# Performance work log

Hardware: AMD Instinct MI355X
Metric: run time of the kernel (lower is better)

Reference implementation:

```python
import jax, jax.numpy as jnp
import numpy as np

B, N, HID = 2, 2048, 1024
NH = 16
HD = HID // NH

def setup_inputs() -> dict:
    key = jax.random.key(0)
    ks = jax.random.split(key, 5)
    s = 0.02
    return {
        "hidden_states": jax.random.normal(ks[0], (B, N, HID), jnp.float32),
        "attention_mask": jnp.zeros((B, 1, 1, N), jnp.float32),
        "Wq": jax.random.normal(ks[1], (HID, HID), jnp.float32) * s,
        "bq": jnp.zeros((HID,), jnp.float32),
        "Wk": jax.random.normal(ks[2], (HID, HID), jnp.float32) * s,
        "bk": jnp.zeros((HID,), jnp.float32),
        "Wv": jax.random.normal(ks[3], (HID, HID), jnp.float32) * s,
        "bv": jnp.zeros((HID,), jnp.float32),
    }

def reference(hidden_states, attention_mask, Wq, bq, Wk, bk, Wv, bv):
    b, n, _ = hidden_states.shape
    def split_heads(t):  # [b,n,hid] -> [b,h,n,d]
        return t.reshape(b, n, NH, HD).transpose(0, 2, 1, 3)
    q = split_heads(hidden_states @ Wq.T + bq)
    k = split_heads(hidden_states @ Wk.T + bk)
    v = split_heads(hidden_states @ Wv.T + bv)
    scores = jnp.einsum('bhnd,bhmd->bhnm', q, k) / jnp.sqrt(jnp.float32(HD)).astype(q.dtype)
    scores = scores + attention_mask
    scores = jnp.maximum(scores, jnp.finfo(scores.dtype).min)
    probs = jax.nn.softmax(scores, axis=-1)
    out = jnp.einsum('bhnm,bhmd->bhnd', probs, v)
    return out.transpose(0, 2, 1, 3).reshape(b, n, NH * HD)
```

## Files before the change

### kernel.cpp

```cpp
#include <hip/hip_runtime.h>

typedef unsigned short u16;
typedef unsigned int   u32;
typedef __attribute__((ext_vector_type(8))) short bf16x8;
typedef __attribute__((ext_vector_type(4))) float f32x4;

__device__ __forceinline__ float bf2f(u16 u) { return __uint_as_float(((u32)u) << 16); }
__device__ __forceinline__ u16 f2bf(float f) {
    return (u16)((__float_as_uint(f) + 0x8000u) >> 16);
}
__device__ __forceinline__ void gload16(const void* g, void* l) {
    __builtin_amdgcn_global_load_lds((const __attribute__((address_space(1))) void*)g,
                                     (__attribute__((address_space(3))) void*)l, 16, 0, 0);
}

struct us4 { u16 x, y, z, w; };
__global__ void cvt_all(const float* __restrict__ hs, const float* __restrict__ wq,
                        const float* __restrict__ wk, const float* __restrict__ wv,
                        u16* __restrict__ dst)
{
    int i = blockIdx.x * blockDim.x + threadIdx.x;
    const int stride = gridDim.x * blockDim.x;
    us4* d4 = (us4*)dst;
    for (; i < 1835008; i += stride) {
        const float4* s4;
        int j = i;
        if (j < 1048576)      { s4 = (const float4*)hs; }
        else if (j < 1310720) { s4 = (const float4*)wq; j -= 1048576; }
        else if (j < 1572864) { s4 = (const float4*)wk; j -= 1310720; }
        else                  { s4 = (const float4*)wv; j -= 1572864; }
        float4 v = s4[j];
        us4 o;
        o.x = f2bf(v.x); o.y = f2bf(v.y); o.z = f2bf(v.z); o.w = f2bf(v.w);
        d4[i] = o;
    }
}

__global__ __launch_bounds__(256) void qkv_gemm(
    const u16* __restrict__ hs,
    const u16* __restrict__ Wq, const u16* __restrict__ Wk, const u16* __restrict__ Wv,
    const float* __restrict__ bq, const float* __restrict__ bk, const float* __restrict__ bv,
    u16* __restrict__ oq, u16* __restrict__ ok, u16* __restrict__ ovt)
{
    __shared__ u16 smem[12288];
    u16* sA = smem;
    u16* sB = smem + 4096;

    const int tid  = threadIdx.x;
    const int lane = tid & 63;
    const int wv_  = tid >> 6;
    const int c15  = lane & 15;
    const int q4   = lane >> 4;
    const int rb   = blockIdx.x;
    const int mat  = blockIdx.y >> 3;
    const int cb   = blockIdx.y & 7;

    const u16*   W    = (mat == 0) ? Wq : (mat == 1 ? Wk : Wv);
    const float* bias = (mat == 0) ? bq : (mat == 1 ? bk : bv);

    f32x4 acc[4][2] = {};

    int rA[2], cA[2], rB[4], cB[4];
#pragma unroll
    for (int p = 0; p < 2; ++p) {
        const int ch = p * 256 + tid;
        rA[p] = ch >> 3; cA[p] = ((ch & 7) ^ (rA[p] & 7)) * 8;
    }
#pragma unroll
    for (int p = 0; p < 4; ++p) {
        const int ch = p * 256 + tid;
        rB[p] = ch >> 3; cB[p] = ((ch & 7) ^ (rB[p] & 7)) * 8;
    }
    const u16* gA = hs + (rb * 64) * 1024;
    const u16* gB = W + (cb * 128) * 1024;
    const int swz = c15 & 7;

    for (int kb = 0; kb < 1024; kb += 64) {
        __syncthreads();
#pragma unroll
        for (int p = 0; p < 2; ++p)
            gload16(gA + rA[p] * 1024 + kb + cA[p], sA + (p * 256 + wv_ * 64) * 8);
#pragma unroll
        for (int p = 0; p < 4; ++p)
            gload16(gB + rB[p] * 1024 + kb + cB[p], sB + (p * 256 + wv_ * 64) * 8);
        __syncthreads();

#pragma unroll
        for (int kk = 0; kk < 2; ++kk) {
            const int cpos = ((kk * 4 + q4) ^ swz) * 8;
            bf16x8 af[4], bf[2];
#pragma unroll
            for (int mt = 0; mt < 4; ++mt)
                af[mt] = *(const bf16x8*)(sA + (mt * 16 + c15) * 64 + cpos);
#pragma unroll
            for (int nt = 0; nt < 2; ++nt)
                bf[nt] = *(const bf16x8*)(sB + (wv_ * 32 + nt * 16 + c15) * 64 + cpos);
#pragma unroll
            for (int mt = 0; mt < 4; ++mt)
#pragma unroll
                for (int nt = 0; nt < 2; ++nt)
                    acc[mt][nt] = __builtin_amdgcn_mfma_f32_16x16x32_bf16(
                        af[mt], bf[nt], acc[mt][nt], 0, 0, 0);
        }
    }

    __syncthreads();
    const int hcol = cb * 2 + (wv_ >> 1);
    const int dbase = (wv_ & 1) * 32;
    float bvv[2];
#pragma unroll
    for (int nt = 0; nt < 2; ++nt)
        bvv[nt] = bias[cb * 128 + wv_ * 32 + nt * 16 + c15];

    u16* sc = smem + wv_ * 2560;
    if (mat != 2) {
        u16* dst = (mat == 0) ? oq : ok;
#pragma unroll
        for (int mt = 0; mt < 4; ++mt)
#pragma unroll
            for (int nt = 0; nt < 2; ++nt)
#pragma unroll
                for (int r = 0; r < 4; ++r)
                    sc[(mt * 16 + q4 * 4 + r) * 40 + nt * 16 + c15] =
                        f2bf(acc[mt][nt][r] + bvv[nt]);
#pragma unroll
        for (int i = 0; i < 4; ++i) {
            const int rl = i * 16 + (lane >> 2);
            const int c0 = (lane & 3) * 8;
            bf16x8 vv = *(const bf16x8*)(sc + rl * 40 + c0);
            const int n = rb * 64 + rl;
            const int bb = n >> 11, nn = n & 2047;
            *(bf16x8*)(dst + (((bb * 16 + hcol) * 2048) + nn) * 64 + dbase + c0) = vv;
        }
    } else {
#pragma unroll
        for (int mt = 0; mt < 4; ++mt)
#pragma unroll
            for (int nt = 0; nt < 2; ++nt)
#pragma unroll
                for (int r = 0; r < 4; ++r)
                    sc[(nt * 16 + c15) * 72 + mt * 16 + q4 * 4 + r] =
                        f2bf(acc[mt][nt][r] + bvv[nt]);
#pragma unroll
        for (int i = 0; i < 4; ++i) {
            const int dp = i * 8 + (lane >> 3);
            const int nl = (lane & 7) * 8;
            bf16x8 vv = *(const bf16x8*)(sc + dp * 72 + nl);
            const int n = rb * 64 + nl;
            const int bb = n >> 11, nn = n & 2047;
            *(bf16x8*)(ovt + (((bb * 16 + hcol) * 64) + dbase + dp) * 2048 + nn) = vv;
        }
    }
}

__global__ __launch_bounds__(256) void attn(
    const u16* __restrict__ qm, const u16* __restrict__ km, const u16* __restrict__ vtm,
    const float* __restrict__ mask, float* __restrict__ out)
{
    __shared__ u16 sK[64 * 64];
    __shared__ u16 sVT[64 * 64];
    __shared__ u16 sP[4][32 * 72];

    const int tid = threadIdx.x, lane = tid & 63, w = tid >> 6;
    const int c15 = lane & 15, q4 = lane >> 4;
    const int qt = blockIdx.x;
    const int bh = blockIdx.y;
    const int b = bh >> 4;

    bf16x8 qf[2][2];
    const u16* qbase = qm + (bh * 2048 + qt * 128 + w * 32) * 64;
#pragma unroll
    for (int rt = 0; rt < 2; ++rt)
#pragma unroll
        for (int kt = 0; kt < 2; ++kt)
            qf[rt][kt] = *(const bf16x8*)(qbase + (rt * 16 + c15) * 64 + kt * 32 + q4 * 8);

    float l_acc[2][4] = {};
    f32x4 accO[2][4] = {};

    const u16* kbase  = km  + bh * 2048 * 64;
    const u16* vtbase = vtm + bh * 64 * 2048;

    const int r0 = tid >> 3,         cc0 = ((tid & 7) ^ (r0 & 7)) * 8;
    const int r1 = (256 + tid) >> 3, cc1 = ((tid & 7) ^ (r1 & 7)) * 8;

    for (int it = 0; it < 32; ++it) {
        const int kb = it * 64;
        __syncthreads();

        gload16(kbase + (kb + r0) * 64 + cc0, sK + (w * 64) * 8);
        gload16(kbase + (kb + r1) * 64 + cc1, sK + (256 + w * 64) * 8);
        gload16(vtbase + r0 * 2048 + kb + cc0, sVT + (w * 64) * 8);
        gload16(vtbase + r1 * 2048 + kb + cc1, sVT + (256 + w * 64) * 8);
        __syncthreads();

        float mk[4];
#pragma unroll
        for (int nt = 0; nt < 4; ++nt)
            mk[nt] = mask[b * 2048 + kb + nt * 16 + c15];

        f32x4 accS[2][4] = {};
#pragma unroll
        for (int kt = 0; kt < 2; ++kt) {
            bf16x8 kf[4];
#pragma unroll
            for (int nt = 0; nt < 4; ++nt) {
                const int key = nt * 16 + c15;
                const int cpos = (q4 + 4 * kt) ^ (key & 7);
                kf[nt] = *(const bf16x8*)(sK + key * 64 + cpos * 8);
            }
#pragma unroll
            for (int rt = 0; rt < 2; ++rt)
#pragma unroll
                for (int nt = 0; nt < 4; ++nt)
                    accS[rt][nt] = __builtin_amdgcn_mfma_f32_16x16x32_bf16(
                        qf[rt][kt], kf[nt], accS[rt][nt], 0, 0, 0);
        }

#pragma unroll
        for (int rt = 0; rt < 2; ++rt)
#pragma unroll
            for (int nt = 0; nt < 4; ++nt)
#pragma unroll
                for (int r = 0; r < 4; ++r) {
                    const float p = __expf(fmaf(accS[rt][nt][r], 0.125f, mk[nt]));
                    l_acc[rt][r] += p;
                    sP[w][(rt * 16 + q4 * 4 + r) * 72 + nt * 16 + c15] = f2bf(p);
                }


#pragma unroll
        for (int kt = 0; kt < 2; ++kt) {
            bf16x8 pf[2], vf[4];
#pragma unroll
            for (int rt = 0; rt < 2; ++rt)
                pf[rt] = *(const bf16x8*)(&sP[w][(rt * 16 + c15) * 72 + kt * 32 + q4 * 8]);
#pragma unroll
            for (int nt = 0; nt < 4; ++nt) {
                const int d = nt * 16 + c15;
                const int cpos = (kt * 4 + q4) ^ (d & 7);
                vf[nt] = *(const bf16x8*)(sVT + d * 64 + cpos * 8);
            }
#pragma unroll
            for (int rt = 0; rt < 2; ++rt)
#pragma unroll
                for (int nt = 0; nt < 4; ++nt)
                    accO[rt][nt] = __builtin_amdgcn_mfma_f32_16x16x32_bf16(
                        pf[rt], vf[nt], accO[rt][nt], 0, 0, 0);
        }
    }

#pragma unroll
    for (int off = 1; off < 16; off <<= 1)
#pragma unroll
        for (int rt = 0; rt < 2; ++rt)
#pragma unroll
            for (int r = 0; r < 4; ++r)
                l_acc[rt][r] += __shfl_xor(l_acc[rt][r], off);

    const int h = bh & 15;
#pragma unroll
    for (int rt = 0; rt < 2; ++rt) {
        float inv[4];
#pragma unroll
        for (int r = 0; r < 4; ++r) inv[r] = 1.0f / l_acc[rt][r];
#pragma unroll
        for (int nt = 0; nt < 4; ++nt)
#pragma unroll
            for (int r = 0; r < 4; ++r) {
                const int qrow = qt * 128 + w * 32 + rt * 16 + q4 * 4 + r;
                const int d = nt * 16 + c15;
                out[(b * 2048 + qrow) * 1024 + h * 64 + d] = accO[rt][nt][r] * inv[r];
            }
    }
}

extern "C" void kernel_launch(void* const* d_in, const int* in_sizes, int n_in,
                              void* d_out, int out_size, void* d_ws, size_t ws_size,
                              hipStream_t stream)
{
    const float* hs   = (const float*)d_in[0];
    const float* mask = (const float*)d_in[1];
    const float* Wq   = (const float*)d_in[2];
    const float* bq   = (const float*)d_in[3];
    const float* Wk   = (const float*)d_in[4];
    const float* bk   = (const float*)d_in[5];
    const float* Wv   = (const float*)d_in[6];
    const float* bv   = (const float*)d_in[7];

    u16* ws   = (u16*)d_ws;
    u16* qw   = ws;
    u16* kw   = ws + 4194304;
    u16* vtw  = ws + 8388608;
    u16* hsb  = ws + 12582912;
    u16* wqb  = ws + 16777216;
    u16* wkb  = ws + 17825792;
    u16* wvb  = ws + 18874368;

    cvt_all<<<1024, 256, 0, stream>>>(hs, Wq, Wk, Wv, hsb);

    qkv_gemm<<<dim3(64, 24), 256, 0, stream>>>(hsb, wqb, wkb, wvb, bq, bk, bv, qw, kw, vtw);
    attn<<<dim3(16, 32), 256, 0, stream>>>(qw, kw, vtw, mask, (float*)d_out);
}
```

Measured before the change: 180.5 us.

## Compute transposed scores and feed probabilities to PV MFMA from registers

Computes S^T = K·Q^T so each lane's accumulator output matches the A-operand layout of the PV MFMA. This drops the per-wave sP shared-memory round trip. Probabilities are packed into bf16 registers with the upper half zero-padded, since only 16 keys per tile are used in the 32-wide MFMA. V^T is loaded as 8-byte halves to match. The padding doubles the PV MFMA count relative to useful work, in exchange for removing LDS writes, reads and related stalls. Row sums now need only two cross-lane shuffles plus a broadcast.

```diff
diff --git a/kernel.cpp b/kernel.cpp
--- a/kernel.cpp
+++ b/kernel.cpp
@@ -4,6 +4,7 @@
 typedef unsigned int   u32;
 typedef __attribute__((ext_vector_type(8))) short bf16x8;
 typedef __attribute__((ext_vector_type(4))) float f32x4;
+typedef __attribute__((ext_vector_type(2))) unsigned int u32x2;
 
 __device__ __forceinline__ float bf2f(u16 u) { return __uint_as_float(((u32)u) << 16); }
 __device__ __forceinline__ u16 f2bf(float f) {
@@ -159,7 +160,6 @@
 {
     __shared__ u16 sK[64 * 64];
     __shared__ u16 sVT[64 * 64];
-    __shared__ u16 sP[4][32 * 72];
 
     const int tid = threadIdx.x, lane = tid & 63, w = tid >> 6;
     const int c15 = lane & 15, q4 = lane >> 4;
@@ -175,7 +175,7 @@
         for (int kt = 0; kt < 2; ++kt)
             qf[rt][kt] = *(const bf16x8*)(qbase + (rt * 16 + c15) * 64 + kt * 32 + q4 * 8);
 
-    float l_acc[2][4] = {};
+    float l_acc[2] = {0.f, 0.f};
     f32x4 accO[2][4] = {};
 
     const u16* kbase  = km  + bh * 2048 * 64;
@@ -194,76 +194,82 @@
         gload16(vtbase + r1 * 2048 + kb + cc1, sVT + (256 + w * 64) * 8);
         __syncthreads();
 
-        float mk[4];
-#pragma unroll
-        for (int nt = 0; nt < 4; ++nt)
-            mk[nt] = mask[b * 2048 + kb + nt * 16 + c15];
-
-        f32x4 accS[2][4] = {};
+        float mkv[4][4];
+#pragma unroll
+        for (int ktile = 0; ktile < 4; ++ktile) {
+            float4 m4 = *(const float4*)(mask + b * 2048 + kb + ktile * 16 + q4 * 4);
+            mkv[ktile][0] = m4.x; mkv[ktile][1] = m4.y;
+            mkv[ktile][2] = m4.z; mkv[ktile][3] = m4.w;
+        }
+
+        f32x4 accST[4][2] = {};
 #pragma unroll
         for (int kt = 0; kt < 2; ++kt) {
             bf16x8 kf[4];
 #pragma unroll
-            for (int nt = 0; nt < 4; ++nt) {
-                const int key = nt * 16 + c15;
-                const int cpos = (q4 + 4 * kt) ^ (key & 7);
-                kf[nt] = *(const bf16x8*)(sK + key * 64 + cpos * 8);
+            for (int ktile = 0; ktile < 4; ++ktile) {
+                const int key = ktile * 16 + c15;
+                const int cpos = (kt * 4 + q4) ^ (key & 7);
+                kf[ktile] = *(const bf16x8*)(sK + key * 64 + cpos * 8);
             }
 #pragma unroll
-            for (int rt = 0; rt < 2; ++rt)
-#pragma unroll
-                for (int nt = 0; nt < 4; ++nt)
-                    accS[rt][nt] = __builtin_amdgcn_mfma_f32_16x16x32_bf16(
-                        qf[rt][kt], kf[nt], accS[rt][nt], 0, 0, 0);
-        }
-
-#pragma unroll
-        for (int rt = 0; rt < 2; ++rt)
-#pragma unroll
-            for (int nt = 0; nt < 4; ++nt)
-#pragma unroll
-                for (int r = 0; r < 4; ++r) {
-                    const float p = __expf(fmaf(accS[rt][nt][r], 0.125f, mk[nt]));
-                    l_acc[rt][r] += p;
-                    sP[w][(rt * 16 + q4 * 4 + r) * 72 + nt * 16 + c15] = f2bf(p);
-                }
-
-
-#pragma unroll
-        for (int kt = 0; kt < 2; ++kt) {
-            bf16x8 pf[2], vf[4];
-#pragma unroll
-            for (int rt = 0; rt < 2; ++rt)
-                pf[rt] = *(const bf16x8*)(&sP[w][(rt * 16 + c15) * 72 + kt * 32 + q4 * 8]);
+            for (int ktile = 0; ktile < 4; ++ktile)
+#pragma unroll
+                for (int rt = 0; rt < 2; ++rt)
+                    accST[ktile][rt] = __builtin_amdgcn_mfma_f32_16x16x32_bf16(
+                        kf[ktile], qf[rt][kt], accST[ktile][rt], 0, 0, 0);
+        }
+
+#pragma unroll
+        for (int ktile = 0; ktile < 4; ++ktile) {
+            bf16x8 vB[4];
 #pragma unroll
             for (int nt = 0; nt < 4; ++nt) {
                 const int d = nt * 16 + c15;
-                const int cpos = (kt * 4 + q4) ^ (d & 7);
-                vf[nt] = *(const bf16x8*)(sVT + d * 64 + cpos * 8);
+                const int pc = (ktile * 2 + (q4 >> 1)) ^ (d & 7);
+                u32x2 pr = *(const u32x2*)(sVT + d * 64 + pc * 8 + (q4 & 1) * 4);
+                union { bf16x8 v; u32 u[4]; } t;
+                t.u[0] = pr.x; t.u[1] = pr.y; t.u[2] = 0; t.u[3] = 0;
+                vB[nt] = t.v;
+            }
+            bf16x8 pA[2];
+#pragma unroll
+            for (int rt = 0; rt < 2; ++rt) {
+                u32 a[4];
+#pragma unroll
+                for (int r = 0; r < 4; ++r) {
+                    const float p = __expf(fmaf(accST[ktile][rt][r], 0.125f, mkv[ktile][r]));
+                    l_acc[rt] += p;
+                    a[r] = __float_as_uint(p) + 0x8000u;
+                }
+                union { bf16x8 v; u32 u[4]; } t;
+                t.u[0] = (a[0] >> 16) | (a[1] & 0xFFFF0000u);
+                t.u[1] = (a[2] >> 16) | (a[3] & 0xFFFF0000u);
+                t.u[2] = 0; t.u[3] = 0;
+                pA[rt] = t.v;
             }
 #pragma unroll
             for (int rt = 0; rt < 2; ++rt)
 #pragma unroll
                 for (int nt = 0; nt < 4; ++nt)
                     accO[rt][nt] = __builtin_amdgcn_mfma_f32_16x16x32_bf16(
-                        pf[rt], vf[nt], accO[rt][nt], 0, 0, 0);
-        }
-    }
-
-#pragma unroll
-    for (int off = 1; off < 16; off <<= 1)
-#pragma unroll
-        for (int rt = 0; rt < 2; ++rt)
-#pragma unroll
-            for (int r = 0; r < 4; ++r)
-                l_acc[rt][r] += __shfl_xor(l_acc[rt][r], off);
+                        pA[rt], vB[nt], accO[rt][nt], 0, 0, 0);
+        }
+    }
+
+#pragma unroll
+    for (int rt = 0; rt < 2; ++rt) {
+        l_acc[rt] += __shfl_xor(l_acc[rt], 16);
+        l_acc[rt] += __shfl_xor(l_acc[rt], 32);
+    }
 
     const int h = bh & 15;
 #pragma unroll
     for (int rt = 0; rt < 2; ++rt) {
         float inv[4];
 #pragma unroll
-        for (int r = 0; r < 4; ++r) inv[r] = 1.0f / l_acc[rt][r];
+        for (int r = 0; r < 4; ++r)
+            inv[r] = 1.0f / __shfl(l_acc[rt], q4 * 4 + r);
 #pragma unroll
         for (int nt = 0; nt < 4; ++nt)
 #pragma unroll
```

Result: slower. 197.8 us (+9.6%).
